# Optimization experiments

Hardware: AMD Instinct MI355X
Metric: run time of the kernel (lower is better)

The kernel has to match this reference:

```python
import jax, jax.numpy as jnp
import numpy as np
from jax import lax

E = 16          # num_experts
CAP = 256       # capacity
MAX_IT = 3      # max_iterations
LPF = 2.0       # load_penalty_factor
DTEMP = 2.0     # diversity_temp
MIN_USAGE = 0.05
NC = 10         # num_classes
TC = 256        # trunk_channels
B = 2048
MIN_TOK = max(1, int(B * MIN_USAGE))        # 102
K_STATIC = min(B, max(CAP, MIN_TOK))        # static top-k width per expert claim


def setup_inputs() -> dict:
    key = jax.random.key(0)
    ks = jax.random.split(key, 16)
    d = {}
    d['x'] = jax.random.normal(ks[0], (B, 3, 32, 32), jnp.float32)
    chans = [(3, 32), (32, 64), (64, 128), (128, 256)]
    for i, (ci, co) in enumerate(chans, 1):
        d[f'cw{i}'] = jax.random.normal(ks[i], (co, ci, 3, 3), jnp.float32) * (1.0 / np.sqrt(ci * 9))
        d[f'cb{i}'] = jnp.zeros((co,), jnp.float32)
        d[f'g{i}'] = jnp.ones((co,), jnp.float32)
        d[f'be{i}'] = jnp.zeros((co,), jnp.float32)
        d[f'm{i}'] = jnp.zeros((co,), jnp.float32)
        d[f'v{i}'] = jnp.ones((co,), jnp.float32)
    d['gw1'] = jax.random.normal(ks[5], (E, TC, TC // 2), jnp.float32) * 0.05
    d['gb1'] = jnp.zeros((E, TC // 2), jnp.float32)
    d['gw2'] = jax.random.normal(ks[6], (E, TC // 2), jnp.float32) * 0.05
    d['gb2'] = jnp.zeros((E,), jnp.float32)
    d['cls_w'] = jax.random.normal(ks[7], (E, NC, TC), jnp.float32) * 0.01
    d['cls_b'] = jnp.zeros((E, NC), jnp.float32)
    d['usage_ema'] = jnp.ones((E,), jnp.float32) / E
    return d


def _conv_bn_relu(x, w, b, g, beta, m, v):
    y = lax.conv_general_dilated(x, w, (1, 1), 'SAME', dimension_numbers=('NCHW', 'OIHW', 'NCHW'))
    y = y + b[None, :, None, None]
    scale = (g / jnp.sqrt(v + 1e-5))[None, :, None, None]
    return jax.nn.relu((y - m[None, :, None, None]) * scale + beta[None, :, None, None])


def _maxpool2(x):
    return lax.reduce_window(x, -jnp.inf, lax.max, (1, 1, 2, 2), (1, 1, 2, 2), 'VALID')


def _forward(x, cw1, cb1, g1, be1, m1, v1, cw2, cb2, g2, be2, m2, v2,
             cw3, cb3, g3, be3, m3, v3, cw4, cb4, g4, be4, m4, v4,
             gw1, gb1, gw2, gb2, cls_w, cls_b, usage_ema):
    # trunk (eval-mode BN)
    h = _conv_bn_relu(x, cw1, cb1, g1, be1, m1, v1)
    h = _conv_bn_relu(h, cw2, cb2, g2, be2, m2, v2)
    h = _maxpool2(h)
    h = _conv_bn_relu(h, cw3, cb3, g3, be3, m3, v3)
    h = _conv_bn_relu(h, cw4, cb4, g4, be4, m4, v4)
    h = _maxpool2(h)
    feats = h.mean(axis=(2, 3))  # AdaptiveAvgPool2d(1)+Flatten -> [B, TC]

    # per-expert classifier heads
    logits_e = jnp.einsum('bd,ecd->bec', feats, cls_w) + cls_b[None]  # [B,E,NC]
    probs = jax.nn.softmax(logits_e, axis=2)
    ent = -(probs * jnp.log(jnp.clip(probs, 1e-12))).sum(axis=2)      # [B,E]
    confidence = -ent

    # per-expert gates (vectorized over experts); dropout is identity in eval
    hidden = jax.nn.relu(jnp.einsum('bd,edh->beh', feats, gw1) + gb1[None])
    expert_scores = (jnp.einsum('beh,eh->be', hidden, gw2) + gb2[None]) / DTEMP

    routing_scores = 0.6 * expert_scores + 0.4 * confidence - LPF * usage_ema[None]

    # iterative capacity-constrained routing (eval: expert order 0..E-1)
    D = jnp.zeros((B, E), bool)
    loads = jnp.zeros((E,), jnp.float32)
    avail = jnp.ones((B,), bool)
    ranks = jnp.arange(K_STATIC)
    for it in range(MAX_IT):
        # penalty from loads at the START of the iteration
        pscores = routing_scores - (it + 1) * LPF * loads[None]
        for j in range(E):
            sj = jnp.where(avail, pscores[:, j], -jnp.inf)
            vc = avail.sum().astype(jnp.int32)
            rc = jnp.maximum(0, CAP - loads[j].astype(jnp.int32))
            ntc = jnp.where((rc == 0) | (vc == 0), 0,
                            jnp.maximum(jnp.minimum(rc, vc), jnp.minimum(MIN_TOK, vc)))
            _, idx = lax.top_k(sj, K_STATIC)
            take = ranks < ntc
            claimed = jnp.zeros((B,), bool).at[idx].set(take)
            D = D.at[:, j].set(D[:, j] | claimed)
            avail = avail & ~claimed
            loads = loads.at[j].add(ntc.astype(jnp.float32))

    # fallback: sequentially assign leftover tokens to least-loaded of top-3
    def fb(carry, inp):
        Dc, lc = carry
        sc, av, i = inp
        _, t3 = lax.top_k(sc, 3)
        best = t3[jnp.argmin(lc[t3])]
        Dc = Dc.at[i, best].set(Dc[i, best] | av)
        lc = lc.at[best].add(av.astype(jnp.float32))
        return (Dc, lc), None

    (D, loads), _ = lax.scan(fb, (D, loads), (routing_scores, avail, jnp.arange(B)))

    Df = D.astype(jnp.float32)
    active = routing_scores * Df
    active = active - active.max(axis=1, keepdims=True)
    weights = jax.nn.softmax(active + (Df - 1.0) * 1e9, axis=1)
    final_logits = (weights[:, :, None] * logits_e).sum(axis=1)
    return final_logits, routing_scores, D


def reference(x, cw1, cb1, g1, be1, m1, v1, cw2, cb2, g2, be2, m2, v2,
              cw3, cb3, g3, be3, m3, v3, cw4, cb4, g4, be4, m4, v4,
              gw1, gb1, gw2, gb2, cls_w, cls_b, usage_ema):
    return _forward(x, cw1, cb1, g1, be1, m1, v1, cw2, cb2, g2, be2, m2, v2,
                    cw3, cb3, g3, be3, m3, v3, cw4, cb4, g4, be4, m4, v4,
                    gw1, gb1, gw2, gb2, cls_w, cls_b, usage_ema)
```

## Files before the change

kernel.cpp:

```cpp
#include <hip/hip_runtime.h>

typedef __attribute__((ext_vector_type(8))) short short8;
typedef __attribute__((ext_vector_type(4))) float f32x4;

__device__ __forceinline__ unsigned short f2bf(float f) {
  unsigned u = __float_as_uint(f);
  unsigned r = (u + 0x7fffu + ((u >> 16) & 1u)) >> 16;
  return (unsigned short)r;
}
__device__ __forceinline__ float bf2f(unsigned short h) {
  return __uint_as_float(((unsigned)h) << 16);
}

__global__ __launch_bounds__(256) void bnprep_kernel(
    const float* __restrict__ g, const float* __restrict__ be,
    const float* __restrict__ m, const float* __restrict__ v,
    const float* __restrict__ b, float* __restrict__ A, float* __restrict__ C, int n)
{
  int i = blockIdx.x * 256 + threadIdx.x;
  if (i < n) {
    float s = g[i] / sqrtf(v[i] + 1e-5f);
    A[i] = s;
    C[i] = (b[i] - m[i]) * s + be[i];
  }
}

__global__ __launch_bounds__(256) void wprep2_kernel(
    const float* __restrict__ w, unsigned short* __restrict__ wPk, int CO, int CI)
{
  int NCB = CI / 32, NF = CO / 16;
  int total = 9 * NCB * NF * 64;
  int idx = blockIdx.x * 256 + threadIdx.x;
  if (idx >= total) return;
  int lane = idx & 63;
  int unit = idx >> 6;
  int f = unit % NF;
  int cb = (unit / NF) % NCB;
  int s = unit / (NF * NCB);
  int co = f * 16 + (lane & 15);
  int ci0 = cb * 32 + (lane >> 4) * 8;
  long base = (long)unit * 1024 + lane * 8;
  #pragma unroll
  for (int j = 0; j < 8; ++j) {
    float v = w[((long)co * CI + ci0 + j) * 9 + s];
    unsigned short h = f2bf(v);
    unsigned short l = f2bf(v - bf2f(h));
    wPk[base + j] = h;
    wPk[base + 512 + j] = l;
  }
}

__global__ __launch_bounds__(512, 2) void conv12_kernel(
    const float* __restrict__ xin, const float* __restrict__ cw1,
    const float* __restrict__ A1p, const float* __restrict__ C1p,
    const unsigned short* __restrict__ wPk, const float* __restrict__ Ap,
    const float* __restrict__ Cp, unsigned short* __restrict__ outA)
{
  constexpr int TY = 16, TX = 32;
  constexpr int PXW = TX + 2;
  constexpr int PXT = (TY + 2) * PXW;
  constexpr int PLSTR = PXT * 8 + 8;
  constexpr int NF = 4;
  __shared__ alignas(16) unsigned short smem[8 * PLSTR];
  __shared__ alignas(16) float sx[2160];
  __shared__ alignas(16) float sw[864];

  const int nwg = gridDim.x;
  const int orig = blockIdx.x;
  const int q = nwg >> 3, r = nwg & 7;
  const int xcd = orig & 7, pos = orig >> 3;
  const int bx = (xcd < r ? xcd * (q + 1) : r * (q + 1) + (xcd - r) * q) + pos;

  const int img = bx >> 1;
  const int tY0 = (bx & 1) * 16;

  const int tid = threadIdx.x;
  const int lane = tid & 63;
  const int lx = lane & 15, kg = lane >> 4;
  const int w = tid >> 6;

  for (int i = tid; i < 2160; i += 512) {
    int c = i / 720, rem = i - c * 720;
    int yy = rem / 36, xx2 = rem - yy * 36;
    int gy = tY0 + yy - 2, gx = xx2 - 2;
    sx[i] = (gy >= 0 && gy < 32 && gx >= 0 && gx < 32)
            ? xin[(long)img * 3072 + c * 1024 + gy * 32 + gx] : 0.f;
  }
  for (int i = tid; i < 864; i += 512) {
    int co = i & 31, kk = i >> 5;
    sw[kk * 32 + co] = cw1[(long)co * 27 + kk];
  }
  __syncthreads();

  #pragma unroll 1
  for (int p = 0; p < 2; ++p) {
    int px = p * 512 + tid;
    if (px < PXT) {
      int ry = px / PXW, rx = px - ry * PXW;
      int gy = tY0 + ry - 1, gx = rx - 1;
      if (gy >= 0 && gy < 32 && gx >= 0 && gx < 32) {
        #pragma unroll 1
        for (int half = 0; half < 2; ++half) {
          float acc[16];
          #pragma unroll
          for (int j = 0; j < 16; ++j) acc[j] = 0.f;
          #pragma unroll
          for (int c = 0; c < 3; ++c) {
            #pragma unroll
            for (int k = 0; k < 9; ++k) {
              int dy = k / 3, dx = k - 3 * (k / 3);
              float iv = sx[c * 720 + (ry + dy) * 36 + rx + dx];
              const float4* w4 = (const float4*)(sw + (c * 9 + k) * 32 + half * 16);
              #pragma unroll
              for (int q2 = 0; q2 < 4; ++q2) {
                float4 wv = w4[q2];
                acc[4 * q2 + 0] += iv * wv.x; acc[4 * q2 + 1] += iv * wv.y;
                acc[4 * q2 + 2] += iv * wv.z; acc[4 * q2 + 3] += iv * wv.w;
              }
            }
          }
          #pragma unroll
          for (int j2 = 0; j2 < 2; ++j2) {
            short8 hv, lv;
            #pragma unroll
            for (int j = 0; j < 8; ++j) {
              int co = half * 16 + j2 * 8 + j;
              float vv = fmaxf(acc[j2 * 8 + j] * A1p[co] + C1p[co], 0.f);
              unsigned short h = f2bf(vv);
              hv[j] = (short)h;
              lv[j] = (short)f2bf(vv - bf2f(h));
            }
            int plane = half * 2 + j2;
            *(short8*)(smem + plane * PLSTR + px * 8) = hv;
            *(short8*)(smem + (plane + 4) * PLSTR + px * 8) = lv;
          }
        }
      } else {
        short8 zz = {0, 0, 0, 0, 0, 0, 0, 0};
        #pragma unroll
        for (int cc = 0; cc < 8; ++cc)
          *(short8*)(smem + cc * PLSTR + px * 8) = zz;
      }
    }
  }
  __syncthreads();

  f32x4 acc[4][4];
  #pragma unroll
  for (int i = 0; i < 4; ++i)
    #pragma unroll
    for (int j = 0; j < 4; ++j) acc[i][j] = (f32x4){0.f, 0.f, 0.f, 0.f};

  for (int s = 0; s < 9; ++s) {
    const int ky = s / 3, kx = s - 3 * (s / 3);
    const long ub = ((long)(s * NF)) * 1024 + lane * 8;
    short8 bh[4], bl[4];
    #pragma unroll
    for (int nf = 0; nf < 4; ++nf) {
      bh[nf] = *(const short8*)(wPk + ub + nf * 1024);
      bl[nf] = *(const short8*)(wPk + ub + nf * 1024 + 512);
    }
    #pragma unroll
    for (int mf = 0; mf < 4; ++mf) {
      const int yoff = mf >> 1;
      const int xb = (mf & 1) * 16;
      const int y = w * 2 + yoff;
      const int pxa = (y + ky) * PXW + xb + kx + lx;
      short8 ah = *(const short8*)(smem + kg * PLSTR + pxa * 8);
      short8 al = *(const short8*)(smem + (kg + 4) * PLSTR + pxa * 8);
      #pragma unroll
      for (int nf = 0; nf < 4; ++nf)
        acc[mf][nf] = __builtin_amdgcn_mfma_f32_16x16x32_bf16(ah, bh[nf], acc[mf][nf], 0, 0, 0);
      #pragma unroll
      for (int nf = 0; nf < 4; ++nf)
        acc[mf][nf] = __builtin_amdgcn_mfma_f32_16x16x32_bf16(ah, bl[nf], acc[mf][nf], 0, 0, 0);
      #pragma unroll
      for (int nf = 0; nf < 4; ++nf)
        acc[mf][nf] = __builtin_amdgcn_mfma_f32_16x16x32_bf16(al, bh[nf], acc[mf][nf], 0, 0, 0);
    }
  }
  __syncthreads();

  float Ar[4], Cr[4];
  #pragma unroll
  for (int nf = 0; nf < 4; ++nf) {
    int co = nf * 16 + lx;
    Ar[nf] = Ap[co]; Cr[nf] = Cp[co];
  }

  unsigned short* slice = smem + w * 2048;
  const int py = (tY0 >> 1) + w;
  #pragma unroll
  for (int xf = 0; xf < 2; ++xf) {
    #pragma unroll
    for (int rp = 0; rp < 2; ++rp) {
      int ox = xf * 8 + 2 * kg + rp;
      #pragma unroll
      for (int nf = 0; nf < 4; ++nf) {
        float v0 = fmaxf(fmaxf(acc[xf][nf][2 * rp], acc[xf][nf][2 * rp + 1]),
                         fmaxf(acc[xf + 2][nf][2 * rp], acc[xf + 2][nf][2 * rp + 1]));
        float vv = fmaxf(v0 * Ar[nf] + Cr[nf], 0.f);
        unsigned short h = f2bf(vv);
        unsigned short l = f2bf(vv - bf2f(h));
        slice[(ox * 2 + 0) * 64 + nf * 16 + lx] = h;
        slice[(ox * 2 + 1) * 64 + nf * 16 + lx] = l;
      }
    }
  }
  #pragma unroll
  for (int v = 0; v < 4; ++v) {
    int hoff = lane * 8 + v * 512;
    int x2 = hoff >> 7, rem = hoff & 127;
    int seg = rem >> 6, inner = rem & 63;
    short8 d = *(const short8*)(slice + hoff);
    *(short8*)(outA + ((long)img * 256 + py * 16 + x2) * 128 + seg * 64 + inner) = d;
  }
}

template<int H, int CI, int CO, int COB, int TY, int TX, int MODE>
__global__ __launch_bounds__(512, 2) void convmf4_kernel(
    const unsigned short* __restrict__ actIn, const unsigned short* __restrict__ wPk,
    const float* __restrict__ Ap, const float* __restrict__ Cp,
    void* __restrict__ outP)
{
  constexpr int NCB = CI / 32;
  constexpr int NF  = CO / 16;
  constexpr int NCOG = COB / 64;
  constexpr int NPXG = 8 / NCOG;
  constexpr int ROWS_PG = TY / NPXG;
  constexpr int FRX = TX / 16;
  constexpr int PXW = TX + 2;
  constexpr int PXT = (TY + 2) * PXW;
  constexpr int PLSTR = PXT * 8 + 8;
  constexpr int TILES_Y = H / TY;
  constexpr int CBLK = CO / COB;
  constexpr int TPI = TILES_Y * CBLK;
  constexpr int PIX_IN = 2 * CI;
  __shared__ alignas(16) unsigned short smem[8 * PLSTR];

  const int nwg = gridDim.x;
  const int orig = blockIdx.x;
  const int q = nwg >> 3, r = nwg & 7;
  const int xcd = orig & 7, pos = orig >> 3;
  const int bx = (xcd < r ? xcd * (q + 1) : r * (q + 1) + (xcd - r) * q) + pos;

  const int img = bx / TPI;
  const int sub = bx % TPI;
  const int tY0 = (sub % TILES_Y) * TY;
  const int blkco = sub / TILES_Y;

  const int tid = threadIdx.x;
  const int lane = tid & 63;
  const int lx = lane & 15, kg = lane >> 4;
  const int w = tid >> 6;
  const int pxg = w % NPXG, cog = w / NPXG;

  f32x4 acc[4][4];
  #pragma unroll
  for (int i = 0; i < 4; ++i)
    #pragma unroll
    for (int j = 0; j < 4; ++j) acc[i][j] = (f32x4){0.f, 0.f, 0.f, 0.f};

  for (int cb = 0; cb < NCB; ++cb) {
    if (cb) __syncthreads();
    for (int t2 = tid; t2 < PXT * 8; t2 += 512) {
      int px = t2 >> 3, c = t2 & 7;
      int ry = px / PXW, rx = px - ry * PXW;
      int gy = tY0 + ry - 1, gx = rx - 1;
      float4 v = (float4){0.f, 0.f, 0.f, 0.f};
      if (gy >= 0 && gy < H && gx >= 0 && gx < H) {
        int coff = (c < 4) ? (cb * 32 + c * 8) : (CI + cb * 32 + (c - 4) * 8);
        v = *(const float4*)(actIn + ((long)img * H * H + gy * H + gx) * PIX_IN + coff);
      }
      *(float4*)(smem + c * PLSTR + px * 8) = v;
    }
    __syncthreads();

    for (int s = 0; s < 9; ++s) {
      const int ky = s / 3, kx = s - 3 * (s / 3);
      const long ub = ((long)(s * NCB + cb) * NF + blkco * (COB / 16) + cog * 4) * 1024
                      + lane * 8;
      short8 bh[4], bl[4];
      #pragma unroll
      for (int nf = 0; nf < 4; ++nf) {
        bh[nf] = *(const short8*)(wPk + ub + nf * 1024);
        bl[nf] = *(const short8*)(wPk + ub + nf * 1024 + 512);
      }
      #pragma unroll
      for (int mf = 0; mf < 4; ++mf) {
        const int yoff = (FRX == 2) ? (mf >> 1) : mf;
        const int xb = (FRX == 2) ? ((mf & 1) * 16) : 0;
        const int y = pxg * ROWS_PG + yoff;
        const int pxa = (y + ky) * PXW + xb + kx + lx;
        short8 ah = *(const short8*)(smem + kg * PLSTR + pxa * 8);
        short8 al = *(const short8*)(smem + (kg + 4) * PLSTR + pxa * 8);
        #pragma unroll
        for (int nf = 0; nf < 4; ++nf)
          acc[mf][nf] = __builtin_amdgcn_mfma_f32_16x16x32_bf16(ah, bh[nf], acc[mf][nf], 0, 0, 0);
        #pragma unroll
        for (int nf = 0; nf < 4; ++nf)
          acc[mf][nf] = __builtin_amdgcn_mfma_f32_16x16x32_bf16(ah, bl[nf], acc[mf][nf], 0, 0, 0);
        #pragma unroll
        for (int nf = 0; nf < 4; ++nf)
          acc[mf][nf] = __builtin_amdgcn_mfma_f32_16x16x32_bf16(al, bh[nf], acc[mf][nf], 0, 0, 0);
      }
    }
  }
  __syncthreads();

  float Ar[4], Cr[4];
  #pragma unroll
  for (int nf = 0; nf < 4; ++nf) {
    int co = blkco * COB + cog * 64 + nf * 16 + lx;
    Ar[nf] = Ap[co]; Cr[nf] = Cp[co];
  }

  if (MODE == 0) {
    unsigned short* outA = (unsigned short*)outP;
    unsigned short* slice = smem + w * 2048;
    #pragma unroll
    for (int mf = 0; mf < 4; ++mf) {
      int y = tY0 + pxg * ROWS_PG + mf;
      #pragma unroll
      for (int rr = 0; rr < 4; ++rr) {
        int x = 4 * kg + rr;
        #pragma unroll
        for (int nf = 0; nf < 4; ++nf) {
          float vv = fmaxf(acc[mf][nf][rr] * Ar[nf] + Cr[nf], 0.f);
          unsigned short h = f2bf(vv);
          unsigned short l = f2bf(vv - bf2f(h));
          slice[(x * 2 + 0) * 64 + nf * 16 + lx] = h;
          slice[(x * 2 + 1) * 64 + nf * 16 + lx] = l;
        }
      }
      #pragma unroll
      for (int v = 0; v < 4; ++v) {
        int hoff = lane * 8 + v * 512;
        int x2 = hoff >> 7, rem = hoff & 127;
        int seg = rem >> 6, inner = rem & 63;
        short8 d = *(const short8*)(slice + hoff);
        *(short8*)(outA + ((long)img * 256 + y * 16 + x2) * (2 * CO)
                   + seg * CO + blkco * COB + cog * 64 + inner) = d;
      }
    }
  } else {
    float psum[4] = {0.f, 0.f, 0.f, 0.f};
    #pragma unroll
    for (int nf = 0; nf < 4; ++nf) {
      #pragma unroll
      for (int mfp = 0; mfp < 2; ++mfp) {
        #pragma unroll
        for (int rp = 0; rp < 2; ++rp) {
          float v = fmaxf(fmaxf(acc[2 * mfp][nf][2 * rp], acc[2 * mfp][nf][2 * rp + 1]),
                          fmaxf(acc[2 * mfp + 1][nf][2 * rp], acc[2 * mfp + 1][nf][2 * rp + 1]));
          psum[nf] += fmaxf(v * Ar[nf] + Cr[nf], 0.f);
        }
      }
    }
    #pragma unroll
    for (int nf = 0; nf < 4; ++nf) {
      psum[nf] += __shfl_xor(psum[nf], 16);
      psum[nf] += __shfl_xor(psum[nf], 32);
    }
    __syncthreads();
    float* sR = (float*)smem;
    if (kg == 0) {
      #pragma unroll
      for (int nf = 0; nf < 4; ++nf) sR[w * 64 + nf * 16 + lx] = psum[nf];
    }
    __syncthreads();
    if (tid < COB) {
      int ct = tid >> 6, ci_ = tid & 63;
      float s = 0.f;
      #pragma unroll
      for (int p = 0; p < NPXG; ++p) s += sR[(ct * NPXG + p) * 64 + ci_];
      ((float*)outP)[(long)img * 256 + blkco * COB + tid] = s * (1.f / 64.f);
    }
  }
}

__global__ __launch_bounds__(512, 1) void convmf5_kernel(
    const unsigned short* __restrict__ actIn, const unsigned short* __restrict__ wPk,
    const float* __restrict__ Ap, const float* __restrict__ Cp,
    float* __restrict__ feats)
{
  constexpr int CI = 128, CO = 256, H = 16;
  constexpr int NCB = 4, NF = 16;
  constexpr int PXW = 18, PXT = 324;
  constexpr int PLSTR = PXT * 8 + 8;
  constexpr int PIX_IN = 2 * CI;
  __shared__ alignas(16) unsigned short smem[8 * PLSTR];

  const int nwg = gridDim.x;
  const int orig = blockIdx.x;
  const int q = nwg >> 3, r = nwg & 7;
  const int xcd = orig & 7, pos = orig >> 3;
  const int img = (xcd < r ? xcd * (q + 1) : r * (q + 1) + (xcd - r) * q) + pos;

  const int tid = threadIdx.x;
  const int lane = tid & 63;
  const int lx = lane & 15, kg = lane >> 4;
  const int w = tid >> 6;
  const int pxg = w >> 1;
  const int cog = w & 1;

  f32x4 acc[4][8];
  #pragma unroll
  for (int i = 0; i < 4; ++i)
    #pragma unroll
    for (int j = 0; j < 8; ++j) acc[i][j] = (f32x4){0.f, 0.f, 0.f, 0.f};

  for (int cb = 0; cb < NCB; ++cb) {
    if (cb) __syncthreads();
    for (int t2 = tid; t2 < PXT * 8; t2 += 512) {
      int px = t2 >> 3, c = t2 & 7;
      int ry = px / PXW, rx = px - ry * PXW;
      int gy = ry - 1, gx = rx - 1;
      float4 v = (float4){0.f, 0.f, 0.f, 0.f};
      if (gy >= 0 && gy < H && gx >= 0 && gx < H) {
        int coff = (c < 4) ? (cb * 32 + c * 8) : (CI + cb * 32 + (c - 4) * 8);
        v = *(const float4*)(actIn + ((long)img * H * H + gy * H + gx) * PIX_IN + coff);
      }
      *(float4*)(smem + c * PLSTR + px * 8) = v;
    }
    __syncthreads();

    for (int s = 0; s < 9; ++s) {
      const int ky = s / 3, kx = s - 3 * (s / 3);
      short8 ah[4], al[4];
      #pragma unroll
      for (int mf = 0; mf < 4; ++mf) {
        const int pxa = (pxg * 4 + mf + ky) * PXW + kx + lx;
        ah[mf] = *(const short8*)(smem + kg * PLSTR + pxa * 8);
        al[mf] = *(const short8*)(smem + (kg + 4) * PLSTR + pxa * 8);
      }
      const long ub = ((long)(s * NCB + cb) * NF + cog * 8) * 1024 + lane * 8;
      {
        short8 bh[4], bl[4];
        #pragma unroll
        for (int nf = 0; nf < 4; ++nf) {
          bh[nf] = *(const short8*)(wPk + ub + nf * 1024);
          bl[nf] = *(const short8*)(wPk + ub + nf * 1024 + 512);
        }
        #pragma unroll
        for (int mf = 0; mf < 4; ++mf) {
          #pragma unroll
          for (int nf = 0; nf < 4; ++nf)
            acc[mf][nf] = __builtin_amdgcn_mfma_f32_16x16x32_bf16(ah[mf], bh[nf], acc[mf][nf], 0, 0, 0);
          #pragma unroll
          for (int nf = 0; nf < 4; ++nf)
            acc[mf][nf] = __builtin_amdgcn_mfma_f32_16x16x32_bf16(ah[mf], bl[nf], acc[mf][nf], 0, 0, 0);
          #pragma unroll
          for (int nf = 0; nf < 4; ++nf)
            acc[mf][nf] = __builtin_amdgcn_mfma_f32_16x16x32_bf16(al[mf], bh[nf], acc[mf][nf], 0, 0, 0);
        }
      }
      {
        short8 bh[4], bl[4];
        #pragma unroll
        for (int nf = 0; nf < 4; ++nf) {
          bh[nf] = *(const short8*)(wPk + ub + (4 + nf) * 1024);
          bl[nf] = *(const short8*)(wPk + ub + (4 + nf) * 1024 + 512);
        }
        #pragma unroll
        for (int mf = 0; mf < 4; ++mf) {
          #pragma unroll
          for (int nf = 0; nf < 4; ++nf)
            acc[mf][4 + nf] = __builtin_amdgcn_mfma_f32_16x16x32_bf16(ah[mf], bh[nf], acc[mf][4 + nf], 0, 0, 0);
          #pragma unroll
          for (int nf = 0; nf < 4; ++nf)
            acc[mf][4 + nf] = __builtin_amdgcn_mfma_f32_16x16x32_bf16(ah[mf], bl[nf], acc[mf][4 + nf], 0, 0, 0);
          #pragma unroll
          for (int nf = 0; nf < 4; ++nf)
            acc[mf][4 + nf] = __builtin_amdgcn_mfma_f32_16x16x32_bf16(al[mf], bh[nf], acc[mf][4 + nf], 0, 0, 0);
        }
      }
    }
  }
  __syncthreads();

  float psum[8];
  #pragma unroll
  for (int j = 0; j < 8; ++j) psum[j] = 0.f;
  #pragma unroll
  for (int j = 0; j < 8; ++j) {
    int co = (cog * 8 + j) * 16 + lx;
    float Ar = Ap[co], Cr = Cp[co];
    #pragma unroll
    for (int u = 0; u < 2; ++u) {
      #pragma unroll
      for (int v = 0; v < 2; ++v) {
        float vm = fmaxf(fmaxf(acc[2 * u][j][2 * v], acc[2 * u][j][2 * v + 1]),
                         fmaxf(acc[2 * u + 1][j][2 * v], acc[2 * u + 1][j][2 * v + 1]));
        psum[j] += fmaxf(vm * Ar + Cr, 0.f);
      }
    }
  }
  #pragma unroll
  for (int j = 0; j < 8; ++j) {
    psum[j] += __shfl_xor(psum[j], 16);
    psum[j] += __shfl_xor(psum[j], 32);
  }
  float* sR = (float*)smem;
  if (kg == 0) {
    #pragma unroll
    for (int j = 0; j < 8; ++j) sR[w * 128 + j * 16 + lx] = psum[j];
  }
  __syncthreads();
  if (tid < 256) {
    int cogT = tid >> 7, cl = tid & 127;
    float s = 0.f;
    #pragma unroll
    for (int p = 0; p < 4; ++p) s += sR[(p * 2 + cogT) * 128 + cl];
    feats[(long)img * 256 + tid] = s * (1.f / 64.f);
  }
}

__global__ __launch_bounds__(256) void heads2_kernel(
    const float* __restrict__ feats, const float* __restrict__ gw1,
    const float* __restrict__ gb1, const float* __restrict__ gw2,
    const float* __restrict__ gb2, const float* __restrict__ clsw,
    const float* __restrict__ clsb, const float* __restrict__ usage,
    float* __restrict__ logits_e, float* __restrict__ rs_out)
{
  __shared__ float sF[64 * 257];
  __shared__ float sLg[4 * 64 * 10];
  __shared__ float sRed[4 * 64];
  const int tid = threadIdx.x;
  const int b0 = blockIdx.x * 64;
  const int e  = blockIdx.y;

  for (int idx = tid; idx < 64 * 64; idx += 256) {
    int t = idx >> 6, dg = idx & 63;
    float4 v = ((const float4*)(feats + (long)(b0 + t) * 256))[dg];
    float* p = sF + t * 257 + dg * 4;
    p[0] = v.x; p[1] = v.y; p[2] = v.z; p[3] = v.w;
  }
  __syncthreads();

  const int t  = tid & 63;
  const int hw = __builtin_amdgcn_readfirstlane(tid >> 6);

  {
    float acc[10];
    #pragma unroll
    for (int c = 0; c < 10; ++c) acc[c] = 0.f;
    const float* fp = sF + t * 257 + hw * 64;
    const float* cw = clsw + (long)e * 2560 + hw * 64;
    for (int dd = 0; dd < 64; ++dd) {
      float f = fp[dd];
      #pragma unroll
      for (int c = 0; c < 10; ++c) acc[c] += f * cw[c * 256 + dd];
    }
    #pragma unroll
    for (int c = 0; c < 10; ++c) sLg[(hw * 64 + t) * 10 + c] = acc[c];
  }
  {
    float gacc[32];
    #pragma unroll
    for (int j = 0; j < 32; ++j) gacc[j] = 0.f;
    const float* wb = gw1 + ((long)e * 256) * 128 + hw * 32;
    const float* fp = sF + t * 257;
    for (int d = 0; d < 256; ++d) {
      float f = fp[d];
      const float4* w4 = (const float4*)(wb + (long)d * 128);
      #pragma unroll
      for (int qq = 0; qq < 8; ++qq) {
        float4 wv = w4[qq];
        gacc[4 * qq + 0] += f * wv.x; gacc[4 * qq + 1] += f * wv.y;
        gacc[4 * qq + 2] += f * wv.z; gacc[4 * qq + 3] += f * wv.w;
      }
    }
    float s = 0.f;
    const float* b1 = gb1 + e * 128 + hw * 32;
    const float* w2 = gw2 + e * 128 + hw * 32;
    #pragma unroll
    for (int j = 0; j < 32; ++j) s += fmaxf(gacc[j] + b1[j], 0.f) * w2[j];
    sRed[hw * 64 + t] = s;
  }
  __syncthreads();

  if (tid < 64) {
    float es = (sRed[t] + sRed[64 + t] + sRed[128 + t] + sRed[192 + t] + gb2[e]) * 0.5f;
    float lg[10];
    #pragma unroll
    for (int c = 0; c < 10; ++c)
      lg[c] = sLg[t * 10 + c] + sLg[(64 + t) * 10 + c]
            + sLg[(128 + t) * 10 + c] + sLg[(192 + t) * 10 + c] + clsb[e * 10 + c];
    float mx = lg[0];
    #pragma unroll
    for (int c = 1; c < 10; ++c) mx = fmaxf(mx, lg[c]);
    float S = 0.f, ps[10];
    #pragma unroll
    for (int c = 0; c < 10; ++c) { ps[c] = expf(lg[c] - mx); S += ps[c]; }
    float inv = 1.f / S, ent = 0.f;
    #pragma unroll
    for (int c = 0; c < 10; ++c) { float p = ps[c] * inv; ent -= p * logf(fmaxf(p, 1e-12f)); }
    float rsv = 0.6f * es + 0.4f * (-ent) - 2.0f * usage[e];
    rs_out[(long)(b0 + t) * 16 + e] = rsv;
    #pragma unroll
    for (int c = 0; c < 10; ++c)
      logits_e[((long)(b0 + t) * 16 + e) * 10 + c] = lg[c];
  }
}

__global__ __launch_bounds__(1024) void sort_kernel(
    const float* __restrict__ rs, unsigned* __restrict__ sortedIdx)
{
  __shared__ unsigned long long sk[2048];
  const int e = blockIdx.x;
  const unsigned tid = threadIdx.x;
  for (int i = tid; i < 2048; i += 1024) {
    float f = rs[(long)i * 16 + e];
    unsigned u = __float_as_uint(f);
    u ^= (u >> 31) ? 0xFFFFFFFFu : 0x80000000u;
    sk[i] = ((unsigned long long)(~u) << 32) | (unsigned)i;
  }
  for (unsigned k = 2; k <= 2048; k <<= 1) {
    for (unsigned j = k >> 1; j > 0; j >>= 1) {
      __syncthreads();
      unsigned i = ((tid & ~(j - 1)) << 1) | (tid & (j - 1));
      unsigned p = i | j;
      bool asc = ((i & k) == 0);
      unsigned long long a = sk[i], b = sk[p];
      if ((a > b) == asc) { sk[i] = b; sk[p] = a; }
    }
  }
  __syncthreads();
  for (int i = tid; i < 2048; i += 1024)
    sortedIdx[(long)e * 2048 + i] = (unsigned)(sk[i] & 0xFFFFFFFFull);
}

__global__ __launch_bounds__(64) void routing2_kernel(
    const unsigned* __restrict__ sortedIdx, const float* __restrict__ rs,
    unsigned* __restrict__ dmaskOut)
{
  __shared__ unsigned char sAvail[2048];
  __shared__ unsigned sDm[2048];
  __shared__ int sLoads[16];
  const int lane = threadIdx.x;
  for (int i = lane; i < 2048; i += 64) { sAvail[i] = 1; sDm[i] = 0; }
  if (lane < 16) sLoads[lane] = 0;
  __syncthreads();

  int vc = 2048;
  for (int it = 0; it < 3; ++it) {
    for (int j = 0; j < 16; ++j) {
      int lj = sLoads[j];
      int rc = 256 - lj; if (rc < 0) rc = 0;
      int ntc = 0;
      if (rc > 0 && vc > 0) {
        int a = rc < vc ? rc : vc;
        int b2 = vc < 102 ? vc : 102;
        ntc = a > b2 ? a : b2;
      }
      if (ntc > 0) {
        const unsigned* se = sortedIdx + (long)j * 2048;
        int taken = 0;
        for (int base = 0; base < 2048; base += 64) {
          if (taken >= ntc) break;
          unsigned tok = se[base + lane];
          int fl = sAvail[tok] ? 1 : 0;
          unsigned long long bm = __ballot(fl);
          int pre = taken + __popcll(bm & ((1ull << lane) - 1ull));
          if (fl && pre < ntc) { sAvail[tok] = 0; sDm[tok] |= (1u << j); }
          taken += (int)__popcll(bm);
          __syncthreads();
        }
        if (lane == 0) sLoads[j] = lj + ntc;
        vc -= ntc;
        __syncthreads();
      }
    }
  }

  if (vc > 0) {
    if (lane == 0) {
      for (int i = 0; i < 2048; ++i) {
        if (!sAvail[i]) continue;
        float s0 = -3.4e38f, s1 = s0, s2 = s0; int e0 = 0, e1 = 0, e2 = 0;
        for (int e = 0; e < 16; ++e) {
          float s = rs[i * 16 + e];
          if (s > s0)      { s2 = s1; e2 = e1; s1 = s0; e1 = e0; s0 = s; e0 = e; }
          else if (s > s1) { s2 = s1; e2 = e1; s1 = s;  e1 = e; }
          else if (s > s2) { s2 = s;  e2 = e; }
        }
        int best = e0, bl = sLoads[e0];
        if (sLoads[e1] < bl) { best = e1; bl = sLoads[e1]; }
        if (sLoads[e2] < bl) { best = e2; bl = sLoads[e2]; }
        sDm[i] |= (1u << best);
        sLoads[best] += 1;
      }
    }
    __syncthreads();
  }

  for (int i = lane; i < 2048; i += 64) dmaskOut[i] = sDm[i];
}

__global__ __launch_bounds__(256) void combine_kernel(
    const unsigned* __restrict__ dmask, const float* __restrict__ rs,
    const float* __restrict__ L, float* __restrict__ out, float* __restrict__ Dout)
{
  int i = blockIdx.x * 256 + threadIdx.x;
  if (i >= 2048) return;
  unsigned dm = dmask[i];
  float r[16];
  #pragma unroll
  for (int e = 0; e < 16; ++e) r[e] = rs[i * 16 + e];
  float mx = -3.4e38f;
  #pragma unroll
  for (int e = 0; e < 16; ++e) {
    float v = ((dm >> e) & 1u) ? r[e] : 0.0f;
    mx = fmaxf(mx, v);
  }
  float w[16], S = 0.f;
  #pragma unroll
  for (int e = 0; e < 16; ++e) {
    w[e] = ((dm >> e) & 1u) ? expf(r[e] - mx) : 0.0f;
    S += w[e];
  }
  float inv = 1.f / S;
  #pragma unroll
  for (int c = 0; c < 10; ++c) {
    float a = 0.f;
    #pragma unroll
    for (int e = 0; e < 16; ++e) a += w[e] * L[((long)i * 16 + e) * 10 + c];
    out[i * 10 + c] = a * inv;
  }
  #pragma unroll
  for (int e = 0; e < 16; ++e)
    Dout[(long)i * 16 + e] = ((dm >> e) & 1u) ? 1.0f : 0.0f;
}

extern "C" void kernel_launch(void* const* d_in, const int* in_sizes, int n_in,
                              void* d_out, int out_size, void* d_ws, size_t ws_size,
                              hipStream_t stream)
{
  const float* x    = (const float*)d_in[0];
  const float* cw1  = (const float*)d_in[1];
  const float* cb1  = (const float*)d_in[2];
  const float* g1   = (const float*)d_in[3];
  const float* be1  = (const float*)d_in[4];
  const float* m1   = (const float*)d_in[5];
  const float* v1   = (const float*)d_in[6];
  const float* cw2  = (const float*)d_in[7];
  const float* cb2  = (const float*)d_in[8];
  const float* g2   = (const float*)d_in[9];
  const float* be2  = (const float*)d_in[10];
  const float* m2   = (const float*)d_in[11];
  const float* v2   = (const float*)d_in[12];
  const float* cw3  = (const float*)d_in[13];
  const float* cb3  = (const float*)d_in[14];
  const float* g3   = (const float*)d_in[15];
  const float* be3  = (const float*)d_in[16];
  const float* m3   = (const float*)d_in[17];
  const float* v3   = (const float*)d_in[18];
  const float* cw4  = (const float*)d_in[19];
  const float* cb4  = (const float*)d_in[20];
  const float* g4   = (const float*)d_in[21];
  const float* be4  = (const float*)d_in[22];
  const float* m4   = (const float*)d_in[23];
  const float* v4   = (const float*)d_in[24];
  const float* gw1  = (const float*)d_in[25];
  const float* gb1  = (const float*)d_in[26];
  const float* gw2  = (const float*)d_in[27];
  const float* gb2  = (const float*)d_in[28];
  const float* clsw = (const float*)d_in[29];
  const float* clsb = (const float*)d_in[30];
  const float* usage = (const float*)d_in[31];

  float* out = (float*)d_out;
  float* ws  = (float*)d_ws;

  float* A1 = ws + 0;   float* C1 = ws + 32;
  float* A2 = ws + 64;  float* C2 = ws + 128;
  float* A3 = ws + 192; float* C3 = ws + 320;
  float* A4 = ws + 448; float* C4 = ws + 704;
  float* feats   = ws + 1024;
  float* logitsE = ws + 525312;
  unsigned* sortedIdx = (unsigned*)(ws + 852992);
  unsigned* dmask     = (unsigned*)(ws + 885760);
  unsigned short* wPk2 = (unsigned short*)(ws + 887808);
  unsigned short* wPk3 = (unsigned short*)(ws + 906240);
  unsigned short* wPk4 = (unsigned short*)(ws + 979968);
  const long bufBase = 1274880;

  long wsFloats = (long)(ws_size / 4);
  long availF = wsFloats - bufBase;
  long chunkL = availF / 49152;
  int chunk = (int)(chunkL < 1 ? 1 : (chunkL > 2048 ? 2048 : chunkL));

  bnprep_kernel<<<1, 256, 0, stream>>>(g1, be1, m1, v1, cb1, A1, C1, 32);
  bnprep_kernel<<<1, 256, 0, stream>>>(g2, be2, m2, v2, cb2, A2, C2, 64);
  bnprep_kernel<<<1, 256, 0, stream>>>(g3, be3, m3, v3, cb3, A3, C3, 128);
  bnprep_kernel<<<1, 256, 0, stream>>>(g4, be4, m4, v4, cb4, A4, C4, 256);
  wprep2_kernel<<<(2304 + 255) / 256, 256, 0, stream>>>(cw2, wPk2, 64, 32);
  wprep2_kernel<<<(9216 + 255) / 256, 256, 0, stream>>>(cw3, wPk3, 128, 64);
  wprep2_kernel<<<(36864 + 255) / 256, 256, 0, stream>>>(cw4, wPk4, 256, 128);

  unsigned short* bufA = (unsigned short*)(ws + bufBase);
  unsigned short* bufB = bufA + (long)chunk * 65536;

  for (int ib = 0; ib < 2048; ib += chunk) {
    int n = 2048 - ib; if (n > chunk) n = chunk;
    conv12_kernel<<<dim3(n * 2), 512, 0, stream>>>(
        x + (long)ib * 3072, cw1, A1, C1, wPk2, A2, C2, bufB);
    convmf4_kernel<16, 64, 128, 128, 16, 16, 0>
        <<<dim3(n), 512, 0, stream>>>(bufB, wPk3, A3, C3, bufA);
    convmf5_kernel<<<dim3(n), 512, 0, stream>>>(bufA, wPk4, A4, C4,
                                                feats + (long)ib * 256);
  }

  float* rsOut = out + 20480;
  heads2_kernel<<<dim3(32, 16), 256, 0, stream>>>(feats, gw1, gb1, gw2, gb2,
                                                  clsw, clsb, usage, logitsE, rsOut);
  sort_kernel<<<16, 1024, 0, stream>>>(rsOut, sortedIdx);
  routing2_kernel<<<1, 64, 0, stream>>>(sortedIdx, rsOut, dmask);
  combine_kernel<<<8, 256, 0, stream>>>(dmask, rsOut, logitsE, out, out + 53248);
}
```

Measured before the change: 1.404 ms.

## Fuse conv3 and conv4 into one kernel keeping conv3 output in shared memory

Merges the conv3 and conv4 MFMA kernels into a single per-image kernel. The conv3 result is written in hi/lo bf16 split form into LDS and read directly by conv4, with a zero slot standing in for padding. This removes the global round trip of the conv3 activation and one launch per chunk, and frees workspace so chunks can be larger. In exchange the fused kernel uses a large LDS footprint at one block per CU, and conv3 work is no longer spread across two blocks per CU.

```diff
diff --git a/kernel.cpp b/kernel.cpp
--- a/kernel.cpp
+++ b/kernel.cpp
@@ -217,179 +217,18 @@
   }
 }
 
-template<int H, int CI, int CO, int COB, int TY, int TX, int MODE>
-__global__ __launch_bounds__(512, 2) void convmf4_kernel(
-    const unsigned short* __restrict__ actIn, const unsigned short* __restrict__ wPk,
-    const float* __restrict__ Ap, const float* __restrict__ Cp,
-    void* __restrict__ outP)
-{
-  constexpr int NCB = CI / 32;
-  constexpr int NF  = CO / 16;
-  constexpr int NCOG = COB / 64;
-  constexpr int NPXG = 8 / NCOG;
-  constexpr int ROWS_PG = TY / NPXG;
-  constexpr int FRX = TX / 16;
-  constexpr int PXW = TX + 2;
-  constexpr int PXT = (TY + 2) * PXW;
-  constexpr int PLSTR = PXT * 8 + 8;
-  constexpr int TILES_Y = H / TY;
-  constexpr int CBLK = CO / COB;
-  constexpr int TPI = TILES_Y * CBLK;
-  constexpr int PIX_IN = 2 * CI;
-  __shared__ alignas(16) unsigned short smem[8 * PLSTR];
-
-  const int nwg = gridDim.x;
-  const int orig = blockIdx.x;
-  const int q = nwg >> 3, r = nwg & 7;
-  const int xcd = orig & 7, pos = orig >> 3;
-  const int bx = (xcd < r ? xcd * (q + 1) : r * (q + 1) + (xcd - r) * q) + pos;
-
-  const int img = bx / TPI;
-  const int sub = bx % TPI;
-  const int tY0 = (sub % TILES_Y) * TY;
-  const int blkco = sub / TILES_Y;
-
-  const int tid = threadIdx.x;
-  const int lane = tid & 63;
-  const int lx = lane & 15, kg = lane >> 4;
-  const int w = tid >> 6;
-  const int pxg = w % NPXG, cog = w / NPXG;
-
-  f32x4 acc[4][4];
-  #pragma unroll
-  for (int i = 0; i < 4; ++i)
-    #pragma unroll
-    for (int j = 0; j < 4; ++j) acc[i][j] = (f32x4){0.f, 0.f, 0.f, 0.f};
-
-  for (int cb = 0; cb < NCB; ++cb) {
-    if (cb) __syncthreads();
-    for (int t2 = tid; t2 < PXT * 8; t2 += 512) {
-      int px = t2 >> 3, c = t2 & 7;
-      int ry = px / PXW, rx = px - ry * PXW;
-      int gy = tY0 + ry - 1, gx = rx - 1;
-      float4 v = (float4){0.f, 0.f, 0.f, 0.f};
-      if (gy >= 0 && gy < H && gx >= 0 && gx < H) {
-        int coff = (c < 4) ? (cb * 32 + c * 8) : (CI + cb * 32 + (c - 4) * 8);
-        v = *(const float4*)(actIn + ((long)img * H * H + gy * H + gx) * PIX_IN + coff);
-      }
-      *(float4*)(smem + c * PLSTR + px * 8) = v;
-    }
-    __syncthreads();
-
-    for (int s = 0; s < 9; ++s) {
-      const int ky = s / 3, kx = s - 3 * (s / 3);
-      const long ub = ((long)(s * NCB + cb) * NF + blkco * (COB / 16) + cog * 4) * 1024
-                      + lane * 8;
-      short8 bh[4], bl[4];
-      #pragma unroll
-      for (int nf = 0; nf < 4; ++nf) {
-        bh[nf] = *(const short8*)(wPk + ub + nf * 1024);
-        bl[nf] = *(const short8*)(wPk + ub + nf * 1024 + 512);
-      }
-      #pragma unroll
-      for (int mf = 0; mf < 4; ++mf) {
-        const int yoff = (FRX == 2) ? (mf >> 1) : mf;
-        const int xb = (FRX == 2) ? ((mf & 1) * 16) : 0;
-        const int y = pxg * ROWS_PG + yoff;
-        const int pxa = (y + ky) * PXW + xb + kx + lx;
-        short8 ah = *(const short8*)(smem + kg * PLSTR + pxa * 8);
-        short8 al = *(const short8*)(smem + (kg + 4) * PLSTR + pxa * 8);
-        #pragma unroll
-        for (int nf = 0; nf < 4; ++nf)
-          acc[mf][nf] = __builtin_amdgcn_mfma_f32_16x16x32_bf16(ah, bh[nf], acc[mf][nf], 0, 0, 0);
-        #pragma unroll
-        for (int nf = 0; nf < 4; ++nf)
-          acc[mf][nf] = __builtin_amdgcn_mfma_f32_16x16x32_bf16(ah, bl[nf], acc[mf][nf], 0, 0, 0);
-        #pragma unroll
-        for (int nf = 0; nf < 4; ++nf)
-          acc[mf][nf] = __builtin_amdgcn_mfma_f32_16x16x32_bf16(al, bh[nf], acc[mf][nf], 0, 0, 0);
-      }
-    }
-  }
-  __syncthreads();
-
-  float Ar[4], Cr[4];
-  #pragma unroll
-  for (int nf = 0; nf < 4; ++nf) {
-    int co = blkco * COB + cog * 64 + nf * 16 + lx;
-    Ar[nf] = Ap[co]; Cr[nf] = Cp[co];
-  }
-
-  if (MODE == 0) {
-    unsigned short* outA = (unsigned short*)outP;
-    unsigned short* slice = smem + w * 2048;
-    #pragma unroll
-    for (int mf = 0; mf < 4; ++mf) {
-      int y = tY0 + pxg * ROWS_PG + mf;
-      #pragma unroll
-      for (int rr = 0; rr < 4; ++rr) {
-        int x = 4 * kg + rr;
-        #pragma unroll
-        for (int nf = 0; nf < 4; ++nf) {
-          float vv = fmaxf(acc[mf][nf][rr] * Ar[nf] + Cr[nf], 0.f);
-          unsigned short h = f2bf(vv);
-          unsigned short l = f2bf(vv - bf2f(h));
-          slice[(x * 2 + 0) * 64 + nf * 16 + lx] = h;
-          slice[(x * 2 + 1) * 64 + nf * 16 + lx] = l;
-        }
-      }
-      #pragma unroll
-      for (int v = 0; v < 4; ++v) {
-        int hoff = lane * 8 + v * 512;
-        int x2 = hoff >> 7, rem = hoff & 127;
-        int seg = rem >> 6, inner = rem & 63;
-        short8 d = *(const short8*)(slice + hoff);
-        *(short8*)(outA + ((long)img * 256 + y * 16 + x2) * (2 * CO)
-                   + seg * CO + blkco * COB + cog * 64 + inner) = d;
-      }
-    }
-  } else {
-    float psum[4] = {0.f, 0.f, 0.f, 0.f};
-    #pragma unroll
-    for (int nf = 0; nf < 4; ++nf) {
-      #pragma unroll
-      for (int mfp = 0; mfp < 2; ++mfp) {
-        #pragma unroll
-        for (int rp = 0; rp < 2; ++rp) {
-          float v = fmaxf(fmaxf(acc[2 * mfp][nf][2 * rp], acc[2 * mfp][nf][2 * rp + 1]),
-                          fmaxf(acc[2 * mfp + 1][nf][2 * rp], acc[2 * mfp + 1][nf][2 * rp + 1]));
-          psum[nf] += fmaxf(v * Ar[nf] + Cr[nf], 0.f);
-        }
-      }
-    }
-    #pragma unroll
-    for (int nf = 0; nf < 4; ++nf) {
-      psum[nf] += __shfl_xor(psum[nf], 16);
-      psum[nf] += __shfl_xor(psum[nf], 32);
-    }
-    __syncthreads();
-    float* sR = (float*)smem;
-    if (kg == 0) {
-      #pragma unroll
-      for (int nf = 0; nf < 4; ++nf) sR[w * 64 + nf * 16 + lx] = psum[nf];
-    }
-    __syncthreads();
-    if (tid < COB) {
-      int ct = tid >> 6, ci_ = tid & 63;
-      float s = 0.f;
-      #pragma unroll
-      for (int p = 0; p < NPXG; ++p) s += sR[(ct * NPXG + p) * 64 + ci_];
-      ((float*)outP)[(long)img * 256 + blkco * COB + tid] = s * (1.f / 64.f);
-    }
-  }
-}
-
-__global__ __launch_bounds__(512, 1) void convmf5_kernel(
-    const unsigned short* __restrict__ actIn, const unsigned short* __restrict__ wPk,
-    const float* __restrict__ Ap, const float* __restrict__ Cp,
-    float* __restrict__ feats)
-{
-  constexpr int CI = 128, CO = 256, H = 16;
-  constexpr int NCB = 4, NF = 16;
-  constexpr int PXW = 18, PXT = 324;
-  constexpr int PLSTR = PXT * 8 + 8;
-  constexpr int PIX_IN = 2 * CI;
-  __shared__ alignas(16) unsigned short smem[8 * PLSTR];
+__global__ __launch_bounds__(512, 1) void convmf45_kernel(
+    const unsigned short* __restrict__ act2,
+    const unsigned short* __restrict__ wPk3, const float* __restrict__ A3p,
+    const float* __restrict__ C3p,
+    const unsigned short* __restrict__ wPk4, const float* __restrict__ A4p,
+    const float* __restrict__ C4p, float* __restrict__ feats)
+{
+  constexpr int PLSTR3 = 2056;
+  constexpr int ZOFF = 32 * PLSTR3;
+  constexpr int PXW2 = 18, PXT2 = 324;
+  constexpr int PLSTR2 = PXT2 * 8 + 8;
+  __shared__ alignas(16) unsigned short smem[ZOFF + 64];
 
   const int nwg = gridDim.x;
   const int orig = blockIdx.x;
@@ -401,6 +240,107 @@
   const int lane = tid & 63;
   const int lx = lane & 15, kg = lane >> 4;
   const int w = tid >> 6;
+
+  if (tid < 8) {
+    short8 zz = {0, 0, 0, 0, 0, 0, 0, 0};
+    *(short8*)(smem + ZOFF + tid * 8) = zz;
+  }
+
+  f32x4 acc3[2][8];
+  #pragma unroll
+  for (int i = 0; i < 2; ++i)
+    #pragma unroll
+    for (int j = 0; j < 8; ++j) acc3[i][j] = (f32x4){0.f, 0.f, 0.f, 0.f};
+
+  for (int cb = 0; cb < 2; ++cb) {
+    __syncthreads();
+    for (int t2 = tid; t2 < PXT2 * 8; t2 += 512) {
+      int px = t2 >> 3, c = t2 & 7;
+      int ry = px / PXW2, rx = px - ry * PXW2;
+      int gy = ry - 1, gx = rx - 1;
+      float4 v = (float4){0.f, 0.f, 0.f, 0.f};
+      if (gy >= 0 && gy < 16 && gx >= 0 && gx < 16) {
+        int coff = (c < 4) ? (cb * 32 + c * 8) : (64 + cb * 32 + (c - 4) * 8);
+        v = *(const float4*)(act2 + ((long)img * 256 + gy * 16 + gx) * 128 + coff);
+      }
+      *(float4*)(smem + c * PLSTR2 + px * 8) = v;
+    }
+    __syncthreads();
+
+    for (int s = 0; s < 9; ++s) {
+      const int ky = s / 3, kx = s - 3 * (s / 3);
+      short8 ah[2], al[2];
+      #pragma unroll
+      for (int mf = 0; mf < 2; ++mf) {
+        const int pxa = (w * 2 + mf + ky) * PXW2 + kx + lx;
+        ah[mf] = *(const short8*)(smem + kg * PLSTR2 + pxa * 8);
+        al[mf] = *(const short8*)(smem + (kg + 4) * PLSTR2 + pxa * 8);
+      }
+      const long ub = ((long)(s * 2 + cb) * 8) * 1024 + lane * 8;
+      {
+        short8 bh[4], bl[4];
+        #pragma unroll
+        for (int nf = 0; nf < 4; ++nf) {
+          bh[nf] = *(const short8*)(wPk3 + ub + nf * 1024);
+          bl[nf] = *(const short8*)(wPk3 + ub + nf * 1024 + 512);
+        }
+        #pragma unroll
+        for (int mf = 0; mf < 2; ++mf) {
+          #pragma unroll
+          for (int nf = 0; nf < 4; ++nf)
+            acc3[mf][nf] = __builtin_amdgcn_mfma_f32_16x16x32_bf16(ah[mf], bh[nf], acc3[mf][nf], 0, 0, 0);
+          #pragma unroll
+          for (int nf = 0; nf < 4; ++nf)
+            acc3[mf][nf] = __builtin_amdgcn_mfma_f32_16x16x32_bf16(ah[mf], bl[nf], acc3[mf][nf], 0, 0, 0);
+          #pragma unroll
+          for (int nf = 0; nf < 4; ++nf)
+            acc3[mf][nf] = __builtin_amdgcn_mfma_f32_16x16x32_bf16(al[mf], bh[nf], acc3[mf][nf], 0, 0, 0);
+        }
+      }
+      {
+        short8 bh[4], bl[4];
+        #pragma unroll
+        for (int nf = 0; nf < 4; ++nf) {
+          bh[nf] = *(const short8*)(wPk3 + ub + (4 + nf) * 1024);
+          bl[nf] = *(const short8*)(wPk3 + ub + (4 + nf) * 1024 + 512);
+        }
+        #pragma unroll
+        for (int mf = 0; mf < 2; ++mf) {
+          #pragma unroll
+          for (int nf = 0; nf < 4; ++nf)
+            acc3[mf][4 + nf] = __builtin_amdgcn_mfma_f32_16x16x32_bf16(ah[mf], bh[nf], acc3[mf][4 + nf], 0, 0, 0);
+          #pragma unroll
+          for (int nf = 0; nf < 4; ++nf)
+            acc3[mf][4 + nf] = __builtin_amdgcn_mfma_f32_16x16x32_bf16(ah[mf], bl[nf], acc3[mf][4 + nf], 0, 0, 0);
+          #pragma unroll
+          for (int nf = 0; nf < 4; ++nf)
+            acc3[mf][4 + nf] = __builtin_amdgcn_mfma_f32_16x16x32_bf16(al[mf], bh[nf], acc3[mf][4 + nf], 0, 0, 0);
+        }
+      }
+    }
+  }
+  __syncthreads();
+
+  #pragma unroll
+  for (int mf = 0; mf < 2; ++mf) {
+    int y = w * 2 + mf;
+    #pragma unroll
+    for (int rr = 0; rr < 4; ++rr) {
+      int px = y * 16 + 4 * kg + rr;
+      #pragma unroll
+      for (int nf = 0; nf < 8; ++nf) {
+        int co = nf * 16 + lx;
+        float vv = fmaxf(acc3[mf][nf][rr] * A3p[co] + C3p[co], 0.f);
+        unsigned short h = f2bf(vv);
+        unsigned short l = f2bf(vv - bf2f(h));
+        int plane = co >> 3, j = co & 7;
+        smem[plane * PLSTR3 + px * 8 + j] = h;
+        smem[(plane + 16) * PLSTR3 + px * 8 + j] = l;
+      }
+    }
+  }
+  __syncthreads();
+
   const int pxg = w >> 1;
   const int cog = w & 1;
 
@@ -410,37 +350,28 @@
     #pragma unroll
     for (int j = 0; j < 8; ++j) acc[i][j] = (f32x4){0.f, 0.f, 0.f, 0.f};
 
-  for (int cb = 0; cb < NCB; ++cb) {
-    if (cb) __syncthreads();
-    for (int t2 = tid; t2 < PXT * 8; t2 += 512) {
-      int px = t2 >> 3, c = t2 & 7;
-      int ry = px / PXW, rx = px - ry * PXW;
-      int gy = ry - 1, gx = rx - 1;
-      float4 v = (float4){0.f, 0.f, 0.f, 0.f};
-      if (gy >= 0 && gy < H && gx >= 0 && gx < H) {
-        int coff = (c < 4) ? (cb * 32 + c * 8) : (CI + cb * 32 + (c - 4) * 8);
-        v = *(const float4*)(actIn + ((long)img * H * H + gy * H + gx) * PIX_IN + coff);
-      }
-      *(float4*)(smem + c * PLSTR + px * 8) = v;
-    }
-    __syncthreads();
-
+  for (int cb = 0; cb < 4; ++cb) {
     for (int s = 0; s < 9; ++s) {
       const int ky = s / 3, kx = s - 3 * (s / 3);
       short8 ah[4], al[4];
       #pragma unroll
       for (int mf = 0; mf < 4; ++mf) {
-        const int pxa = (pxg * 4 + mf + ky) * PXW + kx + lx;
-        ah[mf] = *(const short8*)(smem + kg * PLSTR + pxa * 8);
-        al[mf] = *(const short8*)(smem + (kg + 4) * PLSTR + pxa * 8);
-      }
-      const long ub = ((long)(s * NCB + cb) * NF + cog * 8) * 1024 + lane * 8;
+        int gy = pxg * 4 + mf + ky - 1;
+        int gxx = lx + kx - 1;
+        bool ok = (gy >= 0) && (gy < 16) && (gxx >= 0) && (gxx < 16);
+        int pxo = (gy * 16 + gxx) * 8;
+        int offH = ok ? ((cb * 4 + kg) * PLSTR3 + pxo) : ZOFF;
+        int offL = ok ? ((16 + cb * 4 + kg) * PLSTR3 + pxo) : ZOFF;
+        ah[mf] = *(const short8*)(smem + offH);
+        al[mf] = *(const short8*)(smem + offL);
+      }
+      const long ub = ((long)(s * 4 + cb) * 16 + cog * 8) * 1024 + lane * 8;
       {
         short8 bh[4], bl[4];
         #pragma unroll
         for (int nf = 0; nf < 4; ++nf) {
-          bh[nf] = *(const short8*)(wPk + ub + nf * 1024);
-          bl[nf] = *(const short8*)(wPk + ub + nf * 1024 + 512);
+          bh[nf] = *(const short8*)(wPk4 + ub + nf * 1024);
+          bl[nf] = *(const short8*)(wPk4 + ub + nf * 1024 + 512);
         }
         #pragma unroll
         for (int mf = 0; mf < 4; ++mf) {
@@ -459,8 +390,8 @@
         short8 bh[4], bl[4];
         #pragma unroll
         for (int nf = 0; nf < 4; ++nf) {
-          bh[nf] = *(const short8*)(wPk + ub + (4 + nf) * 1024);
-          bl[nf] = *(const short8*)(wPk + ub + (4 + nf) * 1024 + 512);
+          bh[nf] = *(const short8*)(wPk4 + ub + (4 + nf) * 1024);
+          bl[nf] = *(const short8*)(wPk4 + ub + (4 + nf) * 1024 + 512);
         }
         #pragma unroll
         for (int mf = 0; mf < 4; ++mf) {
@@ -485,7 +416,7 @@
   #pragma unroll
   for (int j = 0; j < 8; ++j) {
     int co = (cog * 8 + j) * 16 + lx;
-    float Ar = Ap[co], Cr = Cp[co];
+    float Ar = A4p[co], Cr = C4p[co];
     #pragma unroll
     for (int u = 0; u < 2; ++u) {
       #pragma unroll
@@ -788,7 +719,7 @@
 
   long wsFloats = (long)(ws_size / 4);
   long availF = wsFloats - bufBase;
-  long chunkL = availF / 49152;
+  long chunkL = availF / 16384;
   int chunk = (int)(chunkL < 1 ? 1 : (chunkL > 2048 ? 2048 : chunkL));
 
   bnprep_kernel<<<1, 256, 0, stream>>>(g1, be1, m1, v1, cb1, A1, C1, 32);
@@ -799,17 +730,14 @@
   wprep2_kernel<<<(9216 + 255) / 256, 256, 0, stream>>>(cw3, wPk3, 128, 64);
   wprep2_kernel<<<(36864 + 255) / 256, 256, 0, stream>>>(cw4, wPk4, 256, 128);
 
-  unsigned short* bufA = (unsigned short*)(ws + bufBase);
-  unsigned short* bufB = bufA + (long)chunk * 65536;
+  unsigned short* act2buf = (unsigned short*)(ws + bufBase);
 
   for (int ib = 0; ib < 2048; ib += chunk) {
     int n = 2048 - ib; if (n > chunk) n = chunk;
     conv12_kernel<<<dim3(n * 2), 512, 0, stream>>>(
-        x + (long)ib * 3072, cw1, A1, C1, wPk2, A2, C2, bufB);
-    convmf4_kernel<16, 64, 128, 128, 16, 16, 0>
-        <<<dim3(n), 512, 0, stream>>>(bufB, wPk3, A3, C3, bufA);
-    convmf5_kernel<<<dim3(n), 512, 0, stream>>>(bufA, wPk4, A4, C4,
-                                                feats + (long)ib * 256);
+        x + (long)ib * 3072, cw1, A1, C1, wPk2, A2, C2, act2buf);
+    convmf45_kernel<<<dim3(n), 512, 0, stream>>>(
+        act2buf, wPk3, A3, C3, wPk4, A4, C4, feats + (long)ib * 256);
   }
 
   float* rsOut = out + 20480;
```

Result: faster. 1.212 ms (-13.7%).
